# Kernel optimization log

Hardware: AMD Instinct MI355X
Metric: run time of the kernel (lower is better)

## Reference

```python
import jax, jax.numpy as jnp
import numpy as np

EMBD_DIM = 10
VOCAB = 32000
MAX_SEQ = 2048


def setup_inputs() -> dict:
    key = jax.random.key(0)
    ks = jax.random.split(key, 7)
    x = jax.random.randint(ks[0], (4, 2048), 0, VOCAB)
    emb = jax.random.normal(ks[1], (VOCAB, EMBD_DIM), dtype=jnp.float32)
    pos_emb = jax.random.normal(ks[2], (MAX_SEQ, EMBD_DIM), dtype=jnp.float32)
    s = 1.0 / np.sqrt(EMBD_DIM)
    Wq = jax.random.normal(ks[3], (EMBD_DIM, EMBD_DIM), dtype=jnp.float32) * s
    Wk = jax.random.normal(ks[4], (EMBD_DIM, EMBD_DIM), dtype=jnp.float32) * s
    Wv = jax.random.normal(ks[5], (EMBD_DIM, EMBD_DIM), dtype=jnp.float32) * s
    Wo = jax.random.normal(ks[6], (VOCAB, EMBD_DIM), dtype=jnp.float32) * s
    return {"x": x, "emb": emb, "pos_emb": pos_emb, "Wq": Wq, "Wk": Wk, "Wv": Wv, "Wo": Wo}


def reference(x, emb, pos_emb, Wq, Wk, Wv, Wo):
    seq_len = x.shape[-1]
    # token + positional embedding: [B, S, D]
    h = emb[x] + pos_emb[:seq_len][None, :, :]
    # torch Linear (no bias): y = x @ W.T
    Q = h @ Wq.T
    K = h @ Wk.T
    V = h @ Wv.T
    score = jnp.einsum('bsd,btd->bst', Q, K)  # [B, S, S]
    causal = jnp.tril(jnp.ones((seq_len, seq_len), dtype=bool))[None]
    # NOTE: original masks with -1e9 BEFORE dividing by sqrt(d) — keep that order
    score = jnp.where(causal, score, jnp.float32(-1e9))
    score = score / jnp.float32(np.sqrt(EMBD_DIM))
    attn = jax.nn.softmax(score, axis=-1)
    out = jnp.einsum('bst,btd->bsd', attn, V)
    logits = out @ Wo.T  # [B, S, vocab]
    return logits
```

## Files before the change

kernel.cpp:

```cpp
#include <hip/hip_runtime.h>
#include <hip/hip_bf16.h>

typedef __hip_bfloat16 bf16;

#define SEQ   2048
#define DIM   10
#define VOC   32000
#define NROW  8192

__device__ __forceinline__ float bfr(unsigned short u) {
    return __uint_as_float(((unsigned)u) << 16);
}

__global__ void probe_kernel(const unsigned short* __restrict__ raw,
                             int* __restrict__ flag) {
    if (blockIdx.x == 0 && threadIdx.x == 0) {
        int sane = 0;
        for (int i = 0; i < 64; i++) {
            unsigned short u = raw[2 * i];
            int e = (u >> 7) & 0xFF;
            if (u == 0 || (e >= 97 && e <= 157)) sane++;
        }
        *flag = (sane >= 48) ? 1 : 0;
    }
}

__global__ __launch_bounds__(256) void qkv_kernel(
    const int* __restrict__ x, const void* __restrict__ embp,
    const void* __restrict__ posp,
    const void* __restrict__ Wqp, const void* __restrict__ Wkp,
    const void* __restrict__ Wvp, const int* __restrict__ flag,
    float* __restrict__ Q, float* __restrict__ K, float* __restrict__ V) {
    __shared__ float wq[DIM * DIM], wk[DIM * DIM], wv[DIM * DIM];
    const int isbf = *flag;
    int t = threadIdx.x;
    if (t < DIM * DIM) {
        if (isbf) {
            wq[t] = bfr(((const unsigned short*)Wqp)[t]);
            wk[t] = bfr(((const unsigned short*)Wkp)[t]);
            wv[t] = bfr(((const unsigned short*)Wvp)[t]);
        } else {
            wq[t] = ((const float*)Wqp)[t];
            wk[t] = ((const float*)Wkp)[t];
            wv[t] = ((const float*)Wvp)[t];
        }
    }
    __syncthreads();
    int row = blockIdx.x * 256 + t;
    int s = row & (SEQ - 1);
    int tok = x[row];
    float h[DIM];
    if (isbf) {
        const unsigned short* e = (const unsigned short*)embp + (size_t)tok * DIM;
        const unsigned short* p = (const unsigned short*)posp + (size_t)s * DIM;
#pragma unroll
        for (int j = 0; j < DIM; j++) h[j] = bfr(e[j]) + bfr(p[j]);
    } else {
        const float* e = (const float*)embp + (size_t)tok * DIM;
        const float* p = (const float*)posp + (size_t)s * DIM;
#pragma unroll
        for (int j = 0; j < DIM; j++) h[j] = e[j] + p[j];
    }
#pragma unroll
    for (int i = 0; i < DIM; i++) {
        float aq = 0.f, ak = 0.f, av = 0.f;
#pragma unroll
        for (int j = 0; j < DIM; j++) {
            aq += h[j] * wq[i * DIM + j];
            ak += h[j] * wk[i * DIM + j];
            av += h[j] * wv[i * DIM + j];
        }
        Q[row * DIM + i] = aq;
        K[row * DIM + i] = ak;
        V[row * DIM + i] = av;
    }
}

__global__ __launch_bounds__(256) void attn_kernel(
    const float* __restrict__ Q, const float* __restrict__ K,
    const float* __restrict__ V, float* __restrict__ O) {
    int wave = threadIdx.x >> 6;
    int lane = threadIdx.x & 63;
    int row = blockIdx.x * 4 + wave;
    int b = row >> 11;
    int s = row & (SEQ - 1);

    const float* qp = Q + row * DIM;
    float q[DIM];
#pragma unroll
    for (int d = 0; d < DIM; d++) q[d] = qp[d];

    const float scale = 0.3162277660168379f;
    const float* Kb = K + (size_t)(b * SEQ) * DIM;
    const float* Vb = V + (size_t)(b * SEQ) * DIM;

    float sc[32];
#pragma unroll
    for (int i = 0; i < 32; i++) {
        int t = lane + (i << 6);
        const float2* kp = (const float2*)(Kb + t * DIM);
        float2 k0 = kp[0], k1 = kp[1], k2 = kp[2], k3 = kp[3], k4 = kp[4];
        float acc = q[0] * k0.x + q[1] * k0.y + q[2] * k1.x + q[3] * k1.y +
                    q[4] * k2.x + q[5] * k2.y + q[6] * k3.x + q[7] * k3.y +
                    q[8] * k4.x + q[9] * k4.y;
        sc[i] = (t <= s) ? acc * scale : -1e30f;
    }
    float m = sc[0];
#pragma unroll
    for (int i = 1; i < 32; i++) m = fmaxf(m, sc[i]);
#pragma unroll
    for (int off = 32; off; off >>= 1) m = fmaxf(m, __shfl_xor(m, off, 64));

    float sum = 0.f;
    float o[DIM];
#pragma unroll
    for (int d = 0; d < DIM; d++) o[d] = 0.f;
#pragma unroll
    for (int i = 0; i < 32; i++) {
        float p = __expf(sc[i] - m);
        sum += p;
        int t = lane + (i << 6);
        const float2* vp = (const float2*)(Vb + t * DIM);
        float2 v0 = vp[0], v1 = vp[1], v2 = vp[2], v3 = vp[3], v4 = vp[4];
        o[0] += p * v0.x; o[1] += p * v0.y;
        o[2] += p * v1.x; o[3] += p * v1.y;
        o[4] += p * v2.x; o[5] += p * v2.y;
        o[6] += p * v3.x; o[7] += p * v3.y;
        o[8] += p * v4.x; o[9] += p * v4.y;
    }
#pragma unroll
    for (int off = 32; off; off >>= 1) {
        sum += __shfl_xor(sum, off, 64);
#pragma unroll
        for (int d = 0; d < DIM; d++) o[d] += __shfl_xor(o[d], off, 64);
    }
    if (lane == 0) {
        float inv = 1.0f / sum;
#pragma unroll
        for (int d = 0; d < DIM; d++) O[row * DIM + d] = o[d] * inv;
    }
}

#define RPB 8
#define VPT 8
__global__ __launch_bounds__(256) void logits_kernel(
    const float* __restrict__ O, const void* __restrict__ Wop,
    const int* __restrict__ flag, void* __restrict__ outp) {
    __shared__ float hrow[RPB][DIM];
    const int isbf = *flag;
    int t = threadIdx.x;
    if (t < RPB * DIM) {
        int r = t / DIM, d = t - r * DIM;
        hrow[r][d] = O[(size_t)(blockIdx.y * RPB + r) * DIM + d];
    }
    __syncthreads();

    int v0 = blockIdx.x * (256 * VPT) + t * VPT;
    if (v0 >= VOC) return;

    float w[VPT][DIM];
    if (isbf) {
        union { uint4 q[10]; unsigned short us[VPT * DIM]; } wr;
        const uint4* p = (const uint4*)((const unsigned short*)Wop + (size_t)v0 * DIM);
#pragma unroll
        for (int k = 0; k < 10; k++) wr.q[k] = p[k];
#pragma unroll
        for (int j = 0; j < VPT; j++)
#pragma unroll
            for (int d = 0; d < DIM; d++) w[j][d] = bfr(wr.us[j * DIM + d]);
    } else {
        union { float4 q[20]; float f[VPT * DIM]; } wr;
        const float4* p = (const float4*)((const float*)Wop + (size_t)v0 * DIM);
#pragma unroll
        for (int k = 0; k < 20; k++) wr.q[k] = p[k];
#pragma unroll
        for (int j = 0; j < VPT; j++)
#pragma unroll
            for (int d = 0; d < DIM; d++) w[j][d] = wr.f[j * DIM + d];
    }

#pragma unroll
    for (int r = 0; r < RPB; r++) {
        float acc[VPT];
#pragma unroll
        for (int j = 0; j < VPT; j++) acc[j] = 0.f;
#pragma unroll
        for (int d = 0; d < DIM; d++) {
            float h = hrow[r][d];
#pragma unroll
            for (int j = 0; j < VPT; j++) acc[j] += h * w[j][d];
        }
        size_t row = (size_t)blockIdx.y * RPB + r;
        if (isbf) {
            union { uint4 u; bf16 h8[8]; } pk;
#pragma unroll
            for (int j = 0; j < VPT; j++) pk.h8[j] = __float2bfloat16(acc[j]);
            *((uint4*)((bf16*)outp + row * VOC + v0)) = pk.u;
        } else {
            float4 a = make_float4(acc[0], acc[1], acc[2], acc[3]);
            float4 b = make_float4(acc[4], acc[5], acc[6], acc[7]);
            float4* op = (float4*)((float*)outp + row * VOC + v0);
            op[0] = a;
            op[1] = b;
        }
    }
}

extern "C" void kernel_launch(void* const* d_in, const int* in_sizes, int n_in,
                              void* d_out, int out_size, void* d_ws, size_t ws_size,
                              hipStream_t stream) {
    const int* x = (const int*)d_in[0];
    const void* emb = d_in[1];
    const void* pos = d_in[2];
    const void* Wq  = d_in[3];
    const void* Wk  = d_in[4];
    const void* Wv  = d_in[5];
    const void* Wo  = d_in[6];

    int*   flag = (int*)d_ws;
    float* base = (float*)d_ws + 64;
    float* Q = base;
    float* K = base + 81920;
    float* V = base + 163840;
    float* O = Q;

    hipLaunchKernelGGL(probe_kernel, dim3(1), dim3(64), 0, stream,
                       (const unsigned short*)emb, flag);
    hipLaunchKernelGGL(qkv_kernel, dim3(NROW / 256), dim3(256), 0, stream,
                       x, emb, pos, Wq, Wk, Wv, flag, Q, K, V);
    hipLaunchKernelGGL(attn_kernel, dim3(NROW / 4), dim3(256), 0, stream,
                       Q, K, V, O);
    hipLaunchKernelGGL(logits_kernel, dim3(16, NROW / RPB), dim3(256), 0,
                       stream, O, Wo, flag, d_out);
}
```

Before: 1.141 ms.

## Tile K/V through shared memory with causal skip, restructure logits stores, ballot probe

The attention kernel now stages K and V in shared memory in 512-row tiles, transposed to a dimension-major layout. It skips tiles that lie entirely beyond the causal limit of the block's rows. The logits kernel assigns 4 vocab columns per thread and processes 64 rows per block, prefetching the next activation row and writing output with nontemporal stores to reduce cache pollution on the large logits write. The probe kernel uses a wave ballot in place of a serial loop. Risks include added barriers and shared-memory bank conflicts in the transposed staging, and lower write width per thread.

```diff
diff --git a/kernel.cpp b/kernel.cpp
--- a/kernel.cpp
+++ b/kernel.cpp
@@ -2,6 +2,8 @@
 #include <hip/hip_bf16.h>
 
 typedef __hip_bfloat16 bf16;
+typedef float  f4v __attribute__((ext_vector_type(4)));
+typedef unsigned int u2v __attribute__((ext_vector_type(2)));
 
 #define SEQ   2048
 #define DIM   10
@@ -14,15 +16,12 @@
 
 __global__ void probe_kernel(const unsigned short* __restrict__ raw,
                              int* __restrict__ flag) {
-    if (blockIdx.x == 0 && threadIdx.x == 0) {
-        int sane = 0;
-        for (int i = 0; i < 64; i++) {
-            unsigned short u = raw[2 * i];
-            int e = (u >> 7) & 0xFF;
-            if (u == 0 || (e >= 97 && e <= 157)) sane++;
-        }
-        *flag = (sane >= 48) ? 1 : 0;
-    }
+    int lane = threadIdx.x;
+    unsigned short u = raw[2 * lane];
+    int e = (u >> 7) & 0xFF;
+    int sane = (u == 0 || (e >= 97 && e <= 157)) ? 1 : 0;
+    unsigned long long b = __ballot(sane != 0);
+    if (lane == 0) *flag = (__popcll(b) >= 48) ? 1 : 0;
 }
 
 __global__ __launch_bounds__(256) void qkv_kernel(
@@ -76,14 +75,18 @@
     }
 }
 
+#define TK 512
 __global__ __launch_bounds__(256) void attn_kernel(
     const float* __restrict__ Q, const float* __restrict__ K,
     const float* __restrict__ V, float* __restrict__ O) {
-    int wave = threadIdx.x >> 6;
-    int lane = threadIdx.x & 63;
-    int row = blockIdx.x * 4 + wave;
-    int b = row >> 11;
-    int s = row & (SEQ - 1);
+    __shared__ float kv[DIM * TK];
+    const int wave = threadIdx.x >> 6;
+    const int lane = threadIdx.x & 63;
+    const int row = blockIdx.x * 4 + wave;
+    const int b = row >> 11;
+    const int s = row & (SEQ - 1);
+    const int smax = (blockIdx.x * 4 + 3) & (SEQ - 1);
+    const int ntiles = (smax >> 9) + 1;
 
     const float* qp = Q + row * DIM;
     float q[DIM];
@@ -96,15 +99,42 @@
 
     float sc[32];
 #pragma unroll
-    for (int i = 0; i < 32; i++) {
-        int t = lane + (i << 6);
-        const float2* kp = (const float2*)(Kb + t * DIM);
-        float2 k0 = kp[0], k1 = kp[1], k2 = kp[2], k3 = kp[3], k4 = kp[4];
-        float acc = q[0] * k0.x + q[1] * k0.y + q[2] * k1.x + q[3] * k1.y +
-                    q[4] * k2.x + q[5] * k2.y + q[6] * k3.x + q[7] * k3.y +
-                    q[8] * k4.x + q[9] * k4.y;
-        sc[i] = (t <= s) ? acc * scale : -1e30f;
-    }
+    for (int i = 0; i < 32; i++) sc[i] = -1e30f;
+
+#pragma unroll
+    for (int tile = 0; tile < 4; tile++) {
+        if (tile < ntiles) {
+            __syncthreads();
+            const float4* src = (const float4*)(Kb + tile * (TK * DIM));
+#pragma unroll
+            for (int u = 0; u < 5; u++) {
+                int e4 = threadIdx.x + u * 256;
+                float4 f = src[e4];
+                int e = e4 * 4;
+                int r0 = (e    ) / 10, d0 = (e    ) - r0 * 10;
+                int r1 = (e + 1) / 10, d1 = (e + 1) - r1 * 10;
+                int r2 = (e + 2) / 10, d2 = (e + 2) - r2 * 10;
+                int r3 = (e + 3) / 10, d3 = (e + 3) - r3 * 10;
+                kv[d0 * TK + r0] = f.x;
+                kv[d1 * TK + r1] = f.y;
+                kv[d2 * TK + r2] = f.z;
+                kv[d3 * TK + r3] = f.w;
+            }
+            __syncthreads();
+#pragma unroll
+            for (int j = 0; j < 8; j++) {
+                int tl = (j << 6) + lane;
+                int t = tile * TK + tl;
+                float acc = q[0] * kv[0 * TK + tl] + q[1] * kv[1 * TK + tl] +
+                            q[2] * kv[2 * TK + tl] + q[3] * kv[3 * TK + tl] +
+                            q[4] * kv[4 * TK + tl] + q[5] * kv[5 * TK + tl] +
+                            q[6] * kv[6 * TK + tl] + q[7] * kv[7 * TK + tl] +
+                            q[8] * kv[8 * TK + tl] + q[9] * kv[9 * TK + tl];
+                sc[tile * 8 + j] = (t <= s) ? acc * scale : -1e30f;
+            }
+        }
+    }
+
     float m = sc[0];
 #pragma unroll
     for (int i = 1; i < 32; i++) m = fmaxf(m, sc[i]);
@@ -115,18 +145,39 @@
     float o[DIM];
 #pragma unroll
     for (int d = 0; d < DIM; d++) o[d] = 0.f;
-#pragma unroll
-    for (int i = 0; i < 32; i++) {
-        float p = __expf(sc[i] - m);
-        sum += p;
-        int t = lane + (i << 6);
-        const float2* vp = (const float2*)(Vb + t * DIM);
-        float2 v0 = vp[0], v1 = vp[1], v2 = vp[2], v3 = vp[3], v4 = vp[4];
-        o[0] += p * v0.x; o[1] += p * v0.y;
-        o[2] += p * v1.x; o[3] += p * v1.y;
-        o[4] += p * v2.x; o[5] += p * v2.y;
-        o[6] += p * v3.x; o[7] += p * v3.y;
-        o[8] += p * v4.x; o[9] += p * v4.y;
+
+#pragma unroll
+    for (int tile = 0; tile < 4; tile++) {
+        if (tile < ntiles) {
+            __syncthreads();
+            const float4* src = (const float4*)(Vb + tile * (TK * DIM));
+#pragma unroll
+            for (int u = 0; u < 5; u++) {
+                int e4 = threadIdx.x + u * 256;
+                float4 f = src[e4];
+                int e = e4 * 4;
+                int r0 = (e    ) / 10, d0 = (e    ) - r0 * 10;
+                int r1 = (e + 1) / 10, d1 = (e + 1) - r1 * 10;
+                int r2 = (e + 2) / 10, d2 = (e + 2) - r2 * 10;
+                int r3 = (e + 3) / 10, d3 = (e + 3) - r3 * 10;
+                kv[d0 * TK + r0] = f.x;
+                kv[d1 * TK + r1] = f.y;
+                kv[d2 * TK + r2] = f.z;
+                kv[d3 * TK + r3] = f.w;
+            }
+            __syncthreads();
+#pragma unroll
+            for (int j = 0; j < 8; j++) {
+                int tl = (j << 6) + lane;
+                float p = __expf(sc[tile * 8 + j] - m);
+                sum += p;
+                o[0] += p * kv[0 * TK + tl]; o[1] += p * kv[1 * TK + tl];
+                o[2] += p * kv[2 * TK + tl]; o[3] += p * kv[3 * TK + tl];
+                o[4] += p * kv[4 * TK + tl]; o[5] += p * kv[5 * TK + tl];
+                o[6] += p * kv[6 * TK + tl]; o[7] += p * kv[7 * TK + tl];
+                o[8] += p * kv[8 * TK + tl]; o[9] += p * kv[9 * TK + tl];
+            }
+        }
     }
 #pragma unroll
     for (int off = 32; off; off >>= 1) {
@@ -141,67 +192,73 @@
     }
 }
 
-#define RPB 8
-#define VPT 8
+#define LRPB 64
 __global__ __launch_bounds__(256) void logits_kernel(
     const float* __restrict__ O, const void* __restrict__ Wop,
     const int* __restrict__ flag, void* __restrict__ outp) {
-    __shared__ float hrow[RPB][DIM];
     const int isbf = *flag;
-    int t = threadIdx.x;
-    if (t < RPB * DIM) {
-        int r = t / DIM, d = t - r * DIM;
-        hrow[r][d] = O[(size_t)(blockIdx.y * RPB + r) * DIM + d];
-    }
-    __syncthreads();
-
-    int v0 = blockIdx.x * (256 * VPT) + t * VPT;
+    const int t = threadIdx.x;
+    const int v0 = blockIdx.x * 1024 + t * 4;
     if (v0 >= VOC) return;
 
-    float w[VPT][DIM];
+    float w[4][DIM];
     if (isbf) {
-        union { uint4 q[10]; unsigned short us[VPT * DIM]; } wr;
+        union { uint4 q[5]; unsigned short us[4 * DIM]; } wr;
         const uint4* p = (const uint4*)((const unsigned short*)Wop + (size_t)v0 * DIM);
 #pragma unroll
-        for (int k = 0; k < 10; k++) wr.q[k] = p[k];
-#pragma unroll
-        for (int j = 0; j < VPT; j++)
+        for (int k = 0; k < 5; k++) wr.q[k] = p[k];
+#pragma unroll
+        for (int j = 0; j < 4; j++)
 #pragma unroll
             for (int d = 0; d < DIM; d++) w[j][d] = bfr(wr.us[j * DIM + d]);
     } else {
-        union { float4 q[20]; float f[VPT * DIM]; } wr;
+        union { float4 q[10]; float f[4 * DIM]; } wr;
         const float4* p = (const float4*)((const float*)Wop + (size_t)v0 * DIM);
 #pragma unroll
-        for (int k = 0; k < 20; k++) wr.q[k] = p[k];
-#pragma unroll
-        for (int j = 0; j < VPT; j++)
+        for (int k = 0; k < 10; k++) wr.q[k] = p[k];
+#pragma unroll
+        for (int j = 0; j < 4; j++)
 #pragma unroll
             for (int d = 0; d < DIM; d++) w[j][d] = wr.f[j * DIM + d];
     }
 
-#pragma unroll
-    for (int r = 0; r < RPB; r++) {
-        float acc[VPT];
-#pragma unroll
-        for (int j = 0; j < VPT; j++) acc[j] = 0.f;
+    const int r0 = blockIdx.y * LRPB;
+    float h[DIM];
+#pragma unroll
+    for (int d = 0; d < DIM; d++) h[d] = O[(size_t)r0 * DIM + d];
+
+    for (int r = 0; r < LRPB; r++) {
+        const int row = r0 + r;
+        float hn[DIM];
+        if (r + 1 < LRPB) {
+#pragma unroll
+            for (int d = 0; d < DIM; d++) hn[d] = O[(size_t)(row + 1) * DIM + d];
+        }
+        float acc0 = 0.f, acc1 = 0.f, acc2 = 0.f, acc3 = 0.f;
 #pragma unroll
         for (int d = 0; d < DIM; d++) {
-            float h = hrow[r][d];
-#pragma unroll
-            for (int j = 0; j < VPT; j++) acc[j] += h * w[j][d];
-        }
-        size_t row = (size_t)blockIdx.y * RPB + r;
+            acc0 += h[d] * w[0][d];
+            acc1 += h[d] * w[1][d];
+            acc2 += h[d] * w[2][d];
+            acc3 += h[d] * w[3][d];
+        }
         if (isbf) {
-            union { uint4 u; bf16 h8[8]; } pk;
-#pragma unroll
-            for (int j = 0; j < VPT; j++) pk.h8[j] = __float2bfloat16(acc[j]);
-            *((uint4*)((bf16*)outp + row * VOC + v0)) = pk.u;
+            union { u2v u; bf16 h4[4]; } pk;
+            pk.h4[0] = __float2bfloat16(acc0);
+            pk.h4[1] = __float2bfloat16(acc1);
+            pk.h4[2] = __float2bfloat16(acc2);
+            pk.h4[3] = __float2bfloat16(acc3);
+            __builtin_nontemporal_store(
+                pk.u, (u2v*)((bf16*)outp + (size_t)row * VOC + v0));
         } else {
-            float4 a = make_float4(acc[0], acc[1], acc[2], acc[3]);
-            float4 b = make_float4(acc[4], acc[5], acc[6], acc[7]);
-            float4* op = (float4*)((float*)outp + row * VOC + v0);
-            op[0] = a;
-            op[1] = b;
+            f4v a;
+            a.x = acc0; a.y = acc1; a.z = acc2; a.w = acc3;
+            __builtin_nontemporal_store(
+                a, (f4v*)((float*)outp + (size_t)row * VOC + v0));
+        }
+        if (r + 1 < LRPB) {
+#pragma unroll
+            for (int d = 0; d < DIM; d++) h[d] = hn[d];
         }
     }
 }
@@ -230,6 +287,6 @@
                        x, emb, pos, Wq, Wk, Wv, flag, Q, K, V);
     hipLaunchKernelGGL(attn_kernel, dim3(NROW / 4), dim3(256), 0, stream,
                        Q, K, V, O);
-    hipLaunchKernelGGL(logits_kernel, dim3(16, NROW / RPB), dim3(256), 0,
+    hipLaunchKernelGGL(logits_kernel, dim3(32, NROW / LRPB), dim3(256), 0,
                        stream, O, Wo, flag, d_out);
 }
```

Result: faster. 1.074 ms (-5.9%).
